# Optimization experiments

Measured on AMD Instinct MI355X. Metric: run time of the kernel, lower is better.

## Reference

```python
import jax, jax.numpy as jnp
import numpy as np

B, T, H, W = 4, 1024, 27, 48
LOOKUP = 101          # must be odd
OUT_DIM = 128
NBINS = 512           # 8 levels per RGB channel -> 8^3


def setup_inputs() -> dict:
    key = jax.random.key(0)
    k1, k2 = jax.random.split(key, 2)
    frames = jax.random.randint(k1, (B, T, H, W, 3), 0, 256, dtype=jnp.int32)
    # nn.Linear(lookup_window, output_dim): weight [out,in] in torch; store transposed [in,out]
    bound = 1.0 / np.sqrt(LOOKUP)
    fc_w = jax.random.uniform(k2, (LOOKUP, OUT_DIM), jnp.float32, -bound, bound)
    fc_b = jnp.zeros((OUT_DIM,), dtype=jnp.float32)
    return {"frames": frames, "fc_w": fc_w, "fc_b": fc_b}


def _color_histograms(frames):
    b, t, h, w, _ = frames.shape
    flat = frames.reshape(b * t, h * w, 3)
    # bit-pack RGB into 9-bit bin id: (R>>5)<<6 | (G>>5)<<3 | (B>>5)
    bins = ((flat[..., 0] >> 5) << 6) + ((flat[..., 1] >> 5) << 3) + (flat[..., 2] >> 5)
    bins = bins + (jnp.arange(b * t, dtype=jnp.int32) << 9)[:, None]  # per-frame offset
    hist = jax.ops.segment_sum(
        jnp.ones((b * t * h * w,), jnp.float32),
        bins.reshape(-1),
        num_segments=b * t * NBINS,
    ).reshape(b, t, NBINS)
    # F.normalize(p=2, dim=2): x / max(||x||, eps)
    norm = jnp.sqrt(jnp.sum(hist * hist, axis=2, keepdims=True))
    return hist / jnp.maximum(norm, 1e-12)


def reference(frames, fc_w, fc_b):
    x = _color_histograms(frames)             # [b, t, 512]
    b, t, _ = x.shape
    sims = jnp.einsum('bic,bjc->bij', x, x)   # [b, t, t]
    pad = (LOOKUP - 1) // 2
    sims_pad = jnp.pad(sims, ((0, 0), (0, 0), (pad, pad)))  # [b, t, t+L-1]
    # windowed gather: out[b,i,j] = sims_pad[b, i, i+j]
    row = jnp.arange(t)[:, None]                     # [t, 1]
    col = row + jnp.arange(LOOKUP)[None, :]          # [t, L]
    win = sims_pad[:, row, col]                      # [b, t, L]
    return jax.nn.relu(jnp.einsum('btl,lo->bto', win, fc_w) + fc_b)
```

## Files before the change

kernel.cpp:

```cpp
#include <hip/hip_runtime.h>
#include <math.h>

#define NB 4
#define NT 1024
#define NPIX 1296
#define NBINS 512
#define LOOKUP 101
#define PADW 50
#define ODIM 128

typedef _Float16 v2h __attribute__((ext_vector_type(2)));

__device__ inline float dot2(unsigned a, unsigned b, float acc) {
    union U { unsigned u; v2h h; } ua, ub;
    ua.u = a; ub.u = b;
#if __has_builtin(__builtin_amdgcn_fdot2)
    return __builtin_amdgcn_fdot2(ua.h, ub.h, acc, false);
#else
    return acc + (float)ua.h.x * (float)ub.h.x + (float)ua.h.y * (float)ub.h.y;
#endif
}

__global__ __launch_bounds__(256) void hist_kernel(const int* __restrict__ frames,
                                                   unsigned short* __restrict__ X) {
    const int frame = blockIdx.x;
    const int tid = threadIdx.x;
    __shared__ unsigned int hist[NBINS];
    for (int i = tid; i < NBINS; i += 256) hist[i] = 0u;
    __syncthreads();

    const int4* f4 = (const int4*)(frames + (size_t)frame * NPIX * 3);
    for (int g = tid; g < NPIX / 4; g += 256) {
        int4 a = f4[g * 3 + 0];
        int4 b = f4[g * 3 + 1];
        int4 c = f4[g * 3 + 2];
        int v[12] = {a.x, a.y, a.z, a.w, b.x, b.y, b.z, b.w, c.x, c.y, c.z, c.w};
#pragma unroll
        for (int p = 0; p < 4; ++p) {
            int bin = ((v[3 * p] >> 5) << 6) | ((v[3 * p + 1] >> 5) << 3) | (v[3 * p + 2] >> 5);
            atomicAdd(&hist[bin], 1u);
        }
    }
    __syncthreads();

    float local = 0.f;
    for (int i = tid; i < NBINS; i += 256) {
        float h = (float)hist[i];
        local += h * h;
    }
    for (int off = 32; off >= 1; off >>= 1) local += __shfl_xor(local, off, 64);
    __shared__ float wsum[4];
    if ((tid & 63) == 0) wsum[tid >> 6] = local;
    __syncthreads();
    float inv = 1.0f / fmaxf(sqrtf(wsum[0] + wsum[1] + wsum[2] + wsum[3]), 1e-12f);

    unsigned* xrow = (unsigned*)(X + (size_t)frame * NBINS);
    union U { _Float16 h[2]; unsigned u; } pk;
    pk.h[0] = (_Float16)((float)hist[2 * tid] * inv);
    pk.h[1] = (_Float16)((float)hist[2 * tid + 1] * inv);
    xrow[tid] = pk.u;
}

__global__ __launch_bounds__(256) void simsfc_kernel(const unsigned short* __restrict__ X,
                                                     const float* __restrict__ w,
                                                     const float* __restrict__ bias,
                                                     float* __restrict__ out) {
    const int bid = blockIdx.x;
    const int frame = ((bid & 7) << 9) | (bid >> 3);
    const int b = frame >> 10;
    const int t = frame & (NT - 1);
    const int tid = threadIdx.x;
    const int lane = tid & 63;
    const int wv = tid >> 6;
    const int grp = lane >> 4;
    const int kl = lane & 15;

    __shared__ __align__(16) uint4 sx[64];
    __shared__ float win[LOOKUP];
    __shared__ float pad[2][ODIM];

    const uint4* xt = (const uint4*)(X + (size_t)frame * NBINS);
    if (tid < 64) sx[tid] = xt[tid];
    __syncthreads();

    const unsigned short* Xb = X + (size_t)b * NT * NBINS;

    for (int r = 0; r < 7; ++r) {
        const int l = r * 16 + wv * 4 + grp;
        const int j = t + l - PADW;
        const bool valid = (l < LOOKUP) & (j >= 0) & (j < NT);
        const int jc = min(max(j, 0), NT - 1);
        const uint4* xj = (const uint4*)(Xb + (size_t)jc * NBINS);
        float a0 = 0.f, a1 = 0.f;
#pragma unroll
        for (int i = 0; i < 4; ++i) {
            uint4 A = xj[kl + 16 * i];
            uint4 S = sx[kl + 16 * i];
            a0 = dot2(A.x, S.x, a0);
            a1 = dot2(A.y, S.y, a1);
            a0 = dot2(A.z, S.z, a0);
            a1 = dot2(A.w, S.w, a1);
        }
        float s = a0 + a1;
        s += __shfl_xor(s, 1, 64);
        s += __shfl_xor(s, 2, 64);
        s += __shfl_xor(s, 4, 64);
        s += __shfl_xor(s, 8, 64);
        if (kl == 0 && l < LOOKUP) win[l] = valid ? s : 0.f;
    }
    __syncthreads();

    const int ch = tid & 127;
    const int half = tid >> 7;
    float acc = half ? 0.f : bias[ch];
    const int l0 = half ? 51 : 0;
    const int l1 = half ? LOOKUP : 51;
#pragma unroll 4
    for (int l = l0; l < l1; ++l)
        acc = fmaf(win[l], w[l * ODIM + ch], acc);
    pad[half][ch] = acc;
    __syncthreads();
    if (tid < ODIM)
        out[(size_t)frame * ODIM + tid] = fmaxf(pad[0][tid] + pad[1][tid], 0.f);
}

extern "C" void kernel_launch(void* const* d_in, const int* in_sizes, int n_in,
                              void* d_out, int out_size, void* d_ws, size_t ws_size,
                              hipStream_t stream) {
    const int*   frames = (const int*)d_in[0];
    const float* fc_w   = (const float*)d_in[1];
    const float* fc_b   = (const float*)d_in[2];
    float* out = (float*)d_out;

    unsigned short* X = (unsigned short*)d_ws;

    hist_kernel  <<<NB * NT, 256, 0, stream>>>(frames, X);
    simsfc_kernel<<<NB * NT, 256, 0, stream>>>(X, fc_w, fc_b, out);
}
```

Baseline: 115.2 us.

## Tile four frames per block in sims/FC kernel and stream frame loads nontemporally

```diff
diff --git a/kernel.cpp b/kernel.cpp
--- a/kernel.cpp
+++ b/kernel.cpp
@@ -8,8 +8,11 @@
 #define LOOKUP 101
 #define PADW 50
 #define ODIM 128
+#define TT 4
+#define WROWS (TT + 2 * PADW)
 
 typedef _Float16 v2h __attribute__((ext_vector_type(2)));
+typedef int v4i __attribute__((ext_vector_type(4)));
 
 __device__ inline float dot2(unsigned a, unsigned b, float acc) {
     union U { unsigned u; v2h h; } ua, ub;
@@ -29,11 +32,11 @@
     for (int i = tid; i < NBINS; i += 256) hist[i] = 0u;
     __syncthreads();
 
-    const int4* f4 = (const int4*)(frames + (size_t)frame * NPIX * 3);
+    const v4i* f4 = (const v4i*)(frames + (size_t)frame * NPIX * 3);
     for (int g = tid; g < NPIX / 4; g += 256) {
-        int4 a = f4[g * 3 + 0];
-        int4 b = f4[g * 3 + 1];
-        int4 c = f4[g * 3 + 2];
+        v4i a = __builtin_nontemporal_load(&f4[g * 3 + 0]);
+        v4i b = __builtin_nontemporal_load(&f4[g * 3 + 1]);
+        v4i c = __builtin_nontemporal_load(&f4[g * 3 + 2]);
         int v[12] = {a.x, a.y, a.z, a.w, b.x, b.y, b.z, b.w, c.x, c.y, c.z, c.w};
 #pragma unroll
         for (int p = 0; p < 4; ++p) {
@@ -61,67 +64,77 @@
     xrow[tid] = pk.u;
 }
 
-__global__ __launch_bounds__(256) void simsfc_kernel(const unsigned short* __restrict__ X,
-                                                     const float* __restrict__ w,
-                                                     const float* __restrict__ bias,
-                                                     float* __restrict__ out) {
+__global__ __launch_bounds__(256, 4) void simsfc_kernel(const unsigned short* __restrict__ X,
+                                                        const float* __restrict__ w,
+                                                        const float* __restrict__ bias,
+                                                        float* __restrict__ out) {
     const int bid = blockIdx.x;
-    const int frame = ((bid & 7) << 9) | (bid >> 3);
-    const int b = frame >> 10;
-    const int t = frame & (NT - 1);
+    const int tile = ((bid & 7) << 7) | (bid >> 3);
+    const int b = tile >> 8;
+    const int t0 = (tile & 255) * TT;
     const int tid = threadIdx.x;
-    const int lane = tid & 63;
-    const int wv = tid >> 6;
-    const int grp = lane >> 4;
-    const int kl = lane & 15;
+    const int gid = tid >> 4;
+    const int kl = tid & 15;
 
-    __shared__ __align__(16) uint4 sx[64];
-    __shared__ float win[LOOKUP];
-    __shared__ float pad[2][ODIM];
+    __shared__ __align__(16) uint4 st[TT][64];
+    __shared__ float win_s[TT][LOOKUP + 3];
 
-    const uint4* xt = (const uint4*)(X + (size_t)frame * NBINS);
-    if (tid < 64) sx[tid] = xt[tid];
+    const uint4* Xb4 = (const uint4*)(X + (size_t)b * NT * NBINS);
+
+    {
+        int dt = tid >> 6, col = tid & 63;
+        st[dt][col] = Xb4[(size_t)(t0 + dt) * 64 + col];
+    }
+    for (int i = tid; i < TT * (LOOKUP + 3); i += 256) ((float*)win_s)[i] = 0.f;
     __syncthreads();
 
-    const unsigned short* Xb = X + (size_t)b * NT * NBINS;
+    uint4 tA[TT][4];
+#pragma unroll
+    for (int dt = 0; dt < TT; ++dt)
+#pragma unroll
+        for (int i = 0; i < 4; ++i) tA[dt][i] = st[dt][kl + 16 * i];
 
-    for (int r = 0; r < 7; ++r) {
-        const int l = r * 16 + wv * 4 + grp;
-        const int j = t + l - PADW;
-        const bool valid = (l < LOOKUP) & (j >= 0) & (j < NT);
-        const int jc = min(max(j, 0), NT - 1);
-        const uint4* xj = (const uint4*)(Xb + (size_t)jc * NBINS);
-        float a0 = 0.f, a1 = 0.f;
+    for (int it = 0; it < 7; ++it) {
+        const int joff = it * 16 + gid;
+        if (joff >= WROWS) continue;
+        const int j = t0 - PADW + joff;
+        if (j < 0 || j >= NT) continue;
+        uint4 A[4];
+        const uint4* xj = Xb4 + (size_t)j * 64;
 #pragma unroll
-        for (int i = 0; i < 4; ++i) {
-            uint4 A = xj[kl + 16 * i];
-            uint4 S = sx[kl + 16 * i];
-            a0 = dot2(A.x, S.x, a0);
-            a1 = dot2(A.y, S.y, a1);
-            a0 = dot2(A.z, S.z, a0);
-            a1 = dot2(A.w, S.w, a1);
+        for (int i = 0; i < 4; ++i) A[i] = xj[kl + 16 * i];
+#pragma unroll
+        for (int dt = 0; dt < TT; ++dt) {
+            float s = 0.f;
+#pragma unroll
+            for (int i = 0; i < 4; ++i) {
+                s = dot2(A[i].x, tA[dt][i].x, s);
+                s = dot2(A[i].y, tA[dt][i].y, s);
+                s = dot2(A[i].z, tA[dt][i].z, s);
+                s = dot2(A[i].w, tA[dt][i].w, s);
+            }
+            s += __shfl_xor(s, 1, 64);
+            s += __shfl_xor(s, 2, 64);
+            s += __shfl_xor(s, 4, 64);
+            s += __shfl_xor(s, 8, 64);
+            const int l = joff - dt;
+            if (kl == 0 && (unsigned)l <= 100u) win_s[dt][l] = s;
         }
-        float s = a0 + a1;
-        s += __shfl_xor(s, 1, 64);
-        s += __shfl_xor(s, 2, 64);
-        s += __shfl_xor(s, 4, 64);
-        s += __shfl_xor(s, 8, 64);
-        if (kl == 0 && l < LOOKUP) win[l] = valid ? s : 0.f;
     }
     __syncthreads();
 
     const int ch = tid & 127;
-    const int half = tid >> 7;
-    float acc = half ? 0.f : bias[ch];
-    const int l0 = half ? 51 : 0;
-    const int l1 = half ? LOOKUP : 51;
+    const int g2 = tid >> 7;
+    float acc0 = bias[ch], acc1 = acc0;
 #pragma unroll 4
-    for (int l = l0; l < l1; ++l)
-        acc = fmaf(win[l], w[l * ODIM + ch], acc);
-    pad[half][ch] = acc;
-    __syncthreads();
-    if (tid < ODIM)
-        out[(size_t)frame * ODIM + tid] = fmaxf(pad[0][tid] + pad[1][tid], 0.f);
+    for (int l = 0; l < LOOKUP; ++l) {
+        float wv = w[l * ODIM + ch];
+        acc0 = fmaf(win_s[g2][l], wv, acc0);
+        acc1 = fmaf(win_s[g2 + 2][l], wv, acc1);
+    }
+    float* o0 = out + ((size_t)(b * NT + t0 + g2) * ODIM) + ch;
+    o0[0] = fmaxf(acc0, 0.f);
+    o0[2 * ODIM] = fmaxf(acc1, 0.f);
 }
 
 extern "C" void kernel_launch(void* const* d_in, const int* in_sizes, int n_in,
@@ -135,5 +148,5 @@
     unsigned short* X = (unsigned short*)d_ws;
 
     hist_kernel  <<<NB * NT, 256, 0, stream>>>(frames, X);
-    simsfc_kernel<<<NB * NT, 256, 0, stream>>>(X, fc_w, fc_b, out);
+    simsfc_kernel<<<NB * NT / TT, 256, 0, stream>>>(X, fc_w, fc_b, out);
 }
```

After: 123.4 us. +7.1%, slower.
